# Kernel tuning notes

Hardware: AMD Instinct MI355X
Metric: run time of the kernel (lower is better)

## Reference

```python
import jax, jax.numpy as jnp
import numpy as np

N = 30000      # num nodes
E = 960000     # num edges (avg degree 32)
IN_DIM = 2048  # raw input feature dim
N_EMBED = 64
N_HID1 = 32
N_HID2 = 16
NUM_ET = 64    # num edge types (relations)
NUM_BASE = 16  # num bases for basis decomposition


def setup_inputs() -> dict:
    key = jax.random.key(0)
    ks = jax.random.split(key, 14)
    x = jax.random.normal(ks[0], (N, IN_DIM), jnp.float32)
    edge_index = jax.random.randint(ks[1], (2, E), 0, N, dtype=jnp.int32)
    edge_type = jnp.sort(jax.random.randint(ks[2], (E,), 0, NUM_ET, dtype=jnp.int32))
    # range_list[r] = [start, end) of relation r's edges (edge_type is sorted)
    bounds = jnp.searchsorted(edge_type, jnp.arange(NUM_ET + 1, dtype=jnp.int32))
    range_list = jnp.stack([bounds[:-1], bounds[1:]], axis=1)
    x_norm = jax.random.uniform(ks[3], (N,), jnp.float32, 0.5, 1.5)
    s = 0.1  # param init scale
    embed = jax.random.normal(ks[4], (IN_DIM, N_EMBED), jnp.float32)  # .normal_() in reset
    basis1 = jax.random.normal(ks[5], (NUM_BASE, N_EMBED, N_HID1), jnp.float32) * s
    att1 = jax.random.normal(ks[6], (NUM_ET, NUM_BASE), jnp.float32) * s
    root1 = jax.random.normal(ks[7], (N_EMBED, N_HID1), jnp.float32) * s
    bias1 = jnp.zeros((N_HID1,), jnp.float32)
    basis2 = jax.random.normal(ks[8], (NUM_BASE, N_HID1, N_HID2), jnp.float32) * s
    att2 = jax.random.normal(ks[9], (NUM_ET, NUM_BASE), jnp.float32) * s
    root2 = jax.random.normal(ks[10], (N_HID1, N_HID2), jnp.float32) * s
    bias2 = jnp.zeros((N_HID2,), jnp.float32)
    return dict(x=x, edge_index=edge_index, edge_type=edge_type, range_list=range_list,
                x_norm=x_norm, embed=embed, basis1=basis1, att1=att1, root1=root1,
                bias1=bias1, basis2=basis2, att2=att2, root2=root2, bias2=bias2)


def rgcn_layer(x, edge_index, edge_type, basis, att, root, bias):
    # basis-decomposed relation weights: W[r] = sum_b att[r,b] * basis[b]
    W = jnp.einsum('rb,bio->rio', att, basis)            # [R, in, out]
    # transform all nodes under every relation (R small per-relation GEMMs fused)
    H = jnp.einsum('ni,rio->rno', x, W)                  # [R, N, out]
    src, dst = edge_index[0], edge_index[1]
    msg = H[edge_type, src]                              # [E, out] gather per-edge message
    agg = jax.ops.segment_sum(msg, dst, num_segments=x.shape[0])  # scatter-add to targets
    return agg + x @ root + bias


def reference(x, edge_index, edge_type, range_list, x_norm,
              embed, basis1, att1, root1, bias1, basis2, att2, root2, bias2):
    h = (x @ embed) / x_norm[:, None]                    # embed matmul + norm
    h = jax.nn.relu(rgcn_layer(h, edge_index, edge_type, basis1, att1, root1, bias1))
    h = jax.nn.relu(rgcn_layer(h, edge_index, edge_type, basis2, att2, root2, bias2))
    return h
```

## Files before the change

### kernel.cpp

```cpp
#include <hip/hip_runtime.h>
#include <hip/hip_bf16.h>

#define NN   30000
#define EE   960000
#define IND  2048
#define NEMB 64
#define NH1  32
#define NH2  16
#define NET  64
#define NB   16

typedef __bf16 bf8 __attribute__((ext_vector_type(8)));
typedef __bf16 bf4 __attribute__((ext_vector_type(4)));
typedef __bf16 bf2 __attribute__((ext_vector_type(2)));
typedef float  f4  __attribute__((ext_vector_type(4)));

#define AS3 __attribute__((address_space(3)))
#define AS1 __attribute__((address_space(1)))

__device__ __forceinline__ void gll16(const void* g, void* l) {
    __builtin_amdgcn_global_load_lds((const AS1 unsigned int*)g,
                                     (AS3 unsigned int*)l, 16, 0, 0);
}

__device__ __forceinline__ bf8 bf8_zero() {
    bf8 z;
#pragma unroll
    for (int i = 0; i < 8; i++) z[i] = (__bf16)0.0f;
    return z;
}

__global__ __launch_bounds__(256) void k_prep(const float* __restrict__ embed,
                                              const float* __restrict__ basis1,
                                              const float* __restrict__ att1,
                                              const float* __restrict__ basis2,
                                              const float* __restrict__ att2,
                                              __bf16* __restrict__ embT,
                                              __bf16* __restrict__ W1T,
                                              __bf16* __restrict__ W2T) {
    int b = blockIdx.x;
    if (b < 512) {
        int idx = b * 256 + threadIdx.x;
        int n = idx >> 11, k = idx & 2047;
        embT[idx] = (__bf16)embed[k * NEMB + n];
    } else if (b < 576) {
        int r = b - 512;
        __shared__ float a[NB];
        if (threadIdx.x < NB) a[threadIdx.x] = att1[r * NB + threadIdx.x];
        __syncthreads();
        for (int idx = threadIdx.x; idx < NH1 * NEMB; idx += 256) {
            int o = idx >> 6, i = idx & 63;
            float acc = 0.f;
#pragma unroll
            for (int bb = 0; bb < NB; bb++) acc += a[bb] * basis1[(bb * NEMB + i) * NH1 + o];
            W1T[r * (NH1 * NEMB) + idx] = (__bf16)acc;
        }
    } else {
        int r = b - 576;
        __shared__ float a[NB];
        if (threadIdx.x < NB) a[threadIdx.x] = att2[r * NB + threadIdx.x];
        __syncthreads();
        for (int idx = threadIdx.x; idx < NH2 * NH1; idx += 256) {
            int o = idx >> 5, i = idx & 31;
            float acc = 0.f;
#pragma unroll
            for (int bb = 0; bb < NB; bb++) acc += a[bb] * basis2[(bb * NH1 + i) * NH2 + o];
            W2T[r * (NH2 * NH1) + idx] = (__bf16)acc;
        }
    }
}

__global__ __launch_bounds__(256) void k_gemm(const float* __restrict__ x,
                                              const float* __restrict__ xnorm,
                                              const __bf16* __restrict__ embT,
                                              const float* __restrict__ root1,
                                              const float* __restrict__ bias1,
                                              __bf16* __restrict__ h0b,
                                              float* __restrict__ out1) {
    __shared__ __align__(16) float  As[2][32 * 128];
    __shared__ __align__(16) __bf16 Bs[2][64 * 128];
    int t = threadIdx.x;
    int wv = t >> 6, lane = t & 63;
    int l15 = lane & 15, kg = lane >> 4;
    int rowbase = blockIdx.x * 32;
    int half = lane >> 5;
    int bslot = lane & 31;
    int q16 = lane >> 4;
    int slot16 = lane & 15;
    int n = wv * 16 + l15;
    int nswz = (n & 7) << 4;
    int aswz = (l15 & 7) << 4;
    f4 acc0 = (f4)0.0f, acc1 = (f4)0.0f;

    auto STAGE = [&](int c, int buf) {
#pragma unroll
        for (int i = 0; i < 4; i++) {
            int rp = wv * 4 + i;
            int row = rp * 2 + half;
            int grow = rowbase + row;
            if (grow >= NN) grow = NN - 1;
            const char* g = (const char*)x + (size_t)grow * (IND * 4) + c * 512
                          + ((bslot * 16) ^ ((row & 7) << 4));
            gll16(g, (char*)&As[buf][0] + rp * 1024);
        }
#pragma unroll
        for (int i = 0; i < 4; i++) {
            int rp = wv * 4 + i;
            int row = rp * 4 + q16;
            const char* g = (const char*)embT + (size_t)row * (IND * 2) + c * 256
                          + ((slot16 * 16) ^ ((row & 7) << 4));
            gll16(g, (char*)&Bs[buf][0] + rp * 1024);
        }
    };

    STAGE(0, 0);
    for (int c = 0; c < 16; c++) {
        int buf = c & 1;
        if (c < 15) {
            STAGE(c + 1, buf ^ 1);
            asm volatile("s_waitcnt vmcnt(8)" ::: "memory");
        } else {
            asm volatile("s_waitcnt vmcnt(0)" ::: "memory");
        }
        __builtin_amdgcn_s_barrier();
        __builtin_amdgcn_sched_barrier(0);
        const char* bsrow  = (const char*)&Bs[buf][0] + n * 256;
        const char* asrow0 = (const char*)&As[buf][0] + l15 * 512;
        const char* asrow1 = (const char*)&As[buf][0] + (l15 + 16) * 512;
#pragma unroll
        for (int kk = 0; kk < 4; kk++) {
            int aoff = ((kk * 128 + kg * 32) ^ aswz);
            float4 lo0 = *(const float4*)(asrow0 + aoff);
            float4 hi0 = *(const float4*)(asrow0 + (aoff ^ 16));
            float4 lo1 = *(const float4*)(asrow1 + aoff);
            float4 hi1 = *(const float4*)(asrow1 + (aoff ^ 16));
            bf8 b = *(const bf8*)(bsrow + ((kk * 64 + kg * 16) ^ nswz));
            bf8 a0, a1;
            a0[0]=(__bf16)lo0.x; a0[1]=(__bf16)lo0.y; a0[2]=(__bf16)lo0.z; a0[3]=(__bf16)lo0.w;
            a0[4]=(__bf16)hi0.x; a0[5]=(__bf16)hi0.y; a0[6]=(__bf16)hi0.z; a0[7]=(__bf16)hi0.w;
            a1[0]=(__bf16)lo1.x; a1[1]=(__bf16)lo1.y; a1[2]=(__bf16)lo1.z; a1[3]=(__bf16)lo1.w;
            a1[4]=(__bf16)hi1.x; a1[5]=(__bf16)hi1.y; a1[6]=(__bf16)hi1.z; a1[7]=(__bf16)hi1.w;
            acc0 = __builtin_amdgcn_mfma_f32_16x16x32_bf16(a0, b, acc0, 0, 0, 0);
            acc1 = __builtin_amdgcn_mfma_f32_16x16x32_bf16(a1, b, acc1, 0, 0, 0);
        }
        __builtin_amdgcn_sched_barrier(0);
        __builtin_amdgcn_s_barrier();
    }
    __bf16* h0s = (__bf16*)&As[0][0];
#pragma unroll
    for (int j = 0; j < 4; j++) {
        int lr0 = kg * 4 + j, lr1 = lr0 + 16;
        int r0 = rowbase + lr0, r1 = rowbase + lr1;
        float v0 = 0.f, v1 = 0.f;
        if (r0 < NN) v0 = acc0[j] / xnorm[r0];
        if (r1 < NN) v1 = acc1[j] / xnorm[r1];
        __bf16 b0 = (__bf16)v0, b1 = (__bf16)v1;
        if (r0 < NN) h0b[(size_t)r0 * NEMB + n] = b0;
        if (r1 < NN) h0b[(size_t)r1 * NEMB + n] = b1;
        h0s[lr0 * NEMB + n] = b0;
        h0s[lr1 * NEMB + n] = b1;
    }
    __syncthreads();
    {
        int row = t >> 3, c0 = (t & 7) * 4;
        int grow = rowbase + row;
        if (grow < NN) {
            const __bf16* hr = h0s + row * NEMB;
            float4 acc = *(const float4*)(bias1 + c0);
#pragma unroll
            for (int k = 0; k < NEMB; k++) {
                float a = (float)hr[k];
                float4 w = *(const float4*)(root1 + k * NH1 + c0);
                acc.x += a * w.x; acc.y += a * w.y;
                acc.z += a * w.z; acc.w += a * w.w;
            }
            *(float4*)(out1 + (size_t)grow * NH1 + c0) = acc;
        }
    }
}

__global__ __launch_bounds__(256) void k_edge1(const int* __restrict__ ei,
                                               const int* __restrict__ et,
                                               const __bf16* __restrict__ h0b,
                                               const __bf16* __restrict__ W1T,
                                               float* __restrict__ out1) {
    int wave = threadIdx.x >> 6, lane = threadIdx.x & 63;
    int l15 = lane & 15, kg = lane >> 4;
    int wid = blockIdx.x * 4 + wave;
    int er0 = wid * 32 + l15, er1 = er0 + 16;
    int et0v = et[er0],  et1v = et[er1];
    int src0 = ei[er0],  src1 = ei[er1];
    int dst0 = ei[EE + er0], dst1 = ei[EE + er1];
    const __bf16* hp0 = h0b + (size_t)src0 * NEMB + kg * 8;
    const __bf16* hp1 = h0b + (size_t)src1 * NEMB + kg * 8;
    bf8 a00 = *(const bf8*)hp0;
    bf8 a01 = *(const bf8*)(hp0 + 32);
    bf8 a10 = *(const bf8*)hp1;
    bf8 a11 = *(const bf8*)(hp1 + 32);
    bf8 zero = bf8_zero();
#pragma unroll
    for (int b = 0; b < 2; b++) {
        int my_et = b ? et1v : et0v;
        int my_dst = b ? dst1 : dst0;
        bf8 a0 = b ? a10 : a00;
        bf8 a1 = b ? a11 : a01;
        f4 c0 = (f4)0.0f, c1 = (f4)0.0f;
        int pos = 0;
        while (pos < 16) {
            int r = __shfl(my_et, pos);
            unsigned long long bl = __ballot(my_et == r);
            unsigned m16 = (unsigned)(bl & 0xFFFFull);
            int run = __builtin_ctz(~(m16 >> pos));
            int end = pos + run;
            const __bf16* wb = W1T + (size_t)r * (NH1 * NEMB) + (size_t)l15 * NEMB + kg * 8;
            bf8 b00 = *(const bf8*)(wb);
            bf8 b01 = *(const bf8*)(wb + 32);
            bf8 b10 = *(const bf8*)(wb + 16 * NEMB);
            bf8 b11 = *(const bf8*)(wb + 16 * NEMB + 32);
            bool use = (l15 >= pos) && (l15 < end);
            bf8 ua0 = use ? a0 : zero;
            bf8 ua1 = use ? a1 : zero;
            c0 = __builtin_amdgcn_mfma_f32_16x16x32_bf16(ua0, b00, c0, 0, 0, 0);
            c0 = __builtin_amdgcn_mfma_f32_16x16x32_bf16(ua1, b01, c0, 0, 0, 0);
            c1 = __builtin_amdgcn_mfma_f32_16x16x32_bf16(ua0, b10, c1, 0, 0, 0);
            c1 = __builtin_amdgcn_mfma_f32_16x16x32_bf16(ua1, b11, c1, 0, 0, 0);
            pos = end;
        }
#pragma unroll
        for (int j = 0; j < 4; j++) {
            int eidx = kg * 4 + j;
            int dst = __shfl(my_dst, eidx);
            atomicAdd(out1 + (size_t)dst * NH1 + l15,      c0[j]);
            atomicAdd(out1 + (size_t)dst * NH1 + 16 + l15, c1[j]);
        }
    }
}

__global__ __launch_bounds__(256) void k_mid(const float* __restrict__ out1,
                                             const float* __restrict__ root2,
                                             const float* __restrict__ bias2,
                                             __bf16* __restrict__ h1b,
                                             float* __restrict__ out) {
    int t = threadIdx.x;
    int row = blockIdx.x * 16 + (t >> 4);
    int col = t & 15;
    const float* orow = out1 + (size_t)row * NH1;
    float h[NH1];
#pragma unroll
    for (int k = 0; k < NH1; k++) h[k] = fmaxf(orow[k], 0.f);
    bf2 hb;
    hb[0] = (__bf16)h[2 * col];
    hb[1] = (__bf16)h[2 * col + 1];
    *(bf2*)(h1b + (size_t)row * NH1 + 2 * col) = hb;
    float acc = bias2[col];
#pragma unroll
    for (int k = 0; k < NH1; k++) acc += h[k] * root2[k * NH2 + col];
    out[(size_t)row * NH2 + col] = acc;
}

__global__ __launch_bounds__(256) void k_edge2(const int* __restrict__ ei,
                                               const int* __restrict__ et,
                                               const __bf16* __restrict__ h1b,
                                               const __bf16* __restrict__ W2T,
                                               float* __restrict__ out) {
    int wave = threadIdx.x >> 6, lane = threadIdx.x & 63;
    int l15 = lane & 15, kg = lane >> 4;
    int wid = blockIdx.x * 4 + wave;
    int er0 = wid * 32 + l15, er1 = er0 + 16;
    int et0v = et[er0],  et1v = et[er1];
    int src0 = ei[er0],  src1 = ei[er1];
    int dst0 = ei[EE + er0], dst1 = ei[EE + er1];
    bf8 ab0 = *(const bf8*)(h1b + (size_t)src0 * NH1 + kg * 8);
    bf8 ab1 = *(const bf8*)(h1b + (size_t)src1 * NH1 + kg * 8);
    bf8 zero = bf8_zero();
#pragma unroll
    for (int b = 0; b < 2; b++) {
        int my_et = b ? et1v : et0v;
        int my_dst = b ? dst1 : dst0;
        bf8 a = b ? ab1 : ab0;
        f4 c = (f4)0.0f;
        int pos = 0;
        while (pos < 16) {
            int r = __shfl(my_et, pos);
            unsigned long long bl = __ballot(my_et == r);
            unsigned m16 = (unsigned)(bl & 0xFFFFull);
            int run = __builtin_ctz(~(m16 >> pos));
            int end = pos + run;
            bf8 bb = *(const bf8*)(W2T + (size_t)r * (NH2 * NH1) + (size_t)l15 * NH1 + kg * 8);
            bool use = (l15 >= pos) && (l15 < end);
            c = __builtin_amdgcn_mfma_f32_16x16x32_bf16(use ? a : zero, bb, c, 0, 0, 0);
            pos = end;
        }
#pragma unroll
        for (int j = 0; j < 4; j++) {
            int eidx = kg * 4 + j;
            int dst = __shfl(my_dst, eidx);
            atomicAdd(out + (size_t)dst * NH2 + l15, c[j]);
        }
    }
}

__global__ __launch_bounds__(256) void k_relu2(float* __restrict__ o) {
    int i = blockIdx.x * 256 + threadIdx.x;
    if (i >= NN * NH2 / 4) return;
    float4 v = ((float4*)o)[i];
    v.x = fmaxf(v.x, 0.f); v.y = fmaxf(v.y, 0.f);
    v.z = fmaxf(v.z, 0.f); v.w = fmaxf(v.w, 0.f);
    ((float4*)o)[i] = v;
}

extern "C" void kernel_launch(void* const* d_in, const int* in_sizes, int n_in,
                              void* d_out, int out_size, void* d_ws, size_t ws_size,
                              hipStream_t stream) {
    const float* x      = (const float*)d_in[0];
    const int*   ei     = (const int*)d_in[1];
    const int*   et     = (const int*)d_in[2];
    const float* xnorm  = (const float*)d_in[4];
    const float* embed  = (const float*)d_in[5];
    const float* basis1 = (const float*)d_in[6];
    const float* att1   = (const float*)d_in[7];
    const float* root1  = (const float*)d_in[8];
    const float* bias1  = (const float*)d_in[9];
    const float* basis2 = (const float*)d_in[10];
    const float* att2   = (const float*)d_in[11];
    const float* root2  = (const float*)d_in[12];
    const float* bias2  = (const float*)d_in[13];
    float* out = (float*)d_out;

    char* ws = (char*)d_ws;
    __bf16* embT = (__bf16*)(ws + 0);
    __bf16* W1T  = (__bf16*)(ws + 262144);
    __bf16* W2T  = (__bf16*)(ws + 524288);
    __bf16* h0b  = (__bf16*)(ws + 589824);
    float*  out1 = (float*) (ws + 4429824);
    __bf16* h1b  = (__bf16*)(ws + 8269824);

    k_prep <<<640,  256, 0, stream>>>(embed, basis1, att1, basis2, att2, embT, W1T, W2T);
    k_gemm <<<938,  256, 0, stream>>>(x, xnorm, embT, root1, bias1, h0b, out1);
    k_edge1<<<7500, 256, 0, stream>>>(ei, et, h0b, W1T, out1);
    k_mid  <<<1875, 256, 0, stream>>>(out1, root2, bias2, h1b, out);
    k_edge2<<<7500, 256, 0, stream>>>(ei, et, h1b, W2T, out);
    k_relu2<<<469,  256, 0, stream>>>(out);
}
```

Baseline: 255.1 us.

## Merge prep+gemm and mid+edge2+relu into persistent kernels with grid barriers

Fuses the weight-prep and embed GEMM into one persistent kernel of 512 blocks separated by a software grid barrier, and likewise fuses the mid transform, second edge layer and final ReLU into one persistent kernel with two grid barriers. This removes several kernel launches and their inter-kernel gaps. In exchange the GEMM now runs 938 tiles over only 512 blocks, which leaves a tail round, and the spin barrier depends on all 512 blocks being co-resident (launch_bounds 256,2 across 256 CUs). The persistent loops also lower parallelism for the edge phase.

```diff
diff --git a/kernel.cpp b/kernel.cpp
--- a/kernel.cpp
+++ b/kernel.cpp
@@ -9,6 +9,7 @@
 #define NH2  16
 #define NET  64
 #define NB   16
+#define NBLKC 512
 
 typedef __bf16 bf8 __attribute__((ext_vector_type(8)));
 typedef __bf16 bf4 __attribute__((ext_vector_type(4)));
@@ -30,59 +31,72 @@
     return z;
 }
 
-__global__ __launch_bounds__(256) void k_prep(const float* __restrict__ embed,
-                                              const float* __restrict__ basis1,
-                                              const float* __restrict__ att1,
-                                              const float* __restrict__ basis2,
-                                              const float* __restrict__ att2,
-                                              __bf16* __restrict__ embT,
-                                              __bf16* __restrict__ W1T,
-                                              __bf16* __restrict__ W2T) {
-    int b = blockIdx.x;
-    if (b < 512) {
-        int idx = b * 256 + threadIdx.x;
-        int n = idx >> 11, k = idx & 2047;
-        embT[idx] = (__bf16)embed[k * NEMB + n];
-    } else if (b < 576) {
-        int r = b - 512;
-        __shared__ float a[NB];
-        if (threadIdx.x < NB) a[threadIdx.x] = att1[r * NB + threadIdx.x];
-        __syncthreads();
-        for (int idx = threadIdx.x; idx < NH1 * NEMB; idx += 256) {
-            int o = idx >> 6, i = idx & 63;
-            float acc = 0.f;
-#pragma unroll
-            for (int bb = 0; bb < NB; bb++) acc += a[bb] * basis1[(bb * NEMB + i) * NH1 + o];
-            W1T[r * (NH1 * NEMB) + idx] = (__bf16)acc;
-        }
-    } else {
-        int r = b - 576;
-        __shared__ float a[NB];
-        if (threadIdx.x < NB) a[threadIdx.x] = att2[r * NB + threadIdx.x];
-        __syncthreads();
-        for (int idx = threadIdx.x; idx < NH2 * NH1; idx += 256) {
-            int o = idx >> 5, i = idx & 31;
-            float acc = 0.f;
-#pragma unroll
-            for (int bb = 0; bb < NB; bb++) acc += a[bb] * basis2[(bb * NH1 + i) * NH2 + o];
-            W2T[r * (NH2 * NH1) + idx] = (__bf16)acc;
-        }
-    }
-}
-
-__global__ __launch_bounds__(256) void k_gemm(const float* __restrict__ x,
-                                              const float* __restrict__ xnorm,
-                                              const __bf16* __restrict__ embT,
-                                              const float* __restrict__ root1,
-                                              const float* __restrict__ bias1,
-                                              __bf16* __restrict__ h0b,
-                                              float* __restrict__ out1) {
+__device__ __forceinline__ void gridbar(int* bar, int target) {
+    __syncthreads();
+    if (threadIdx.x == 0) {
+        __threadfence();
+        if (atomicAdd(&bar[0], 1) == NBLKC - 1) {
+            bar[0] = 0;
+            __threadfence();
+            atomicAdd(&bar[1], 1);
+        }
+        while (__hip_atomic_load(&bar[1], __ATOMIC_ACQUIRE,
+                                 __HIP_MEMORY_SCOPE_AGENT) < target)
+            __builtin_amdgcn_s_sleep(32);
+        __threadfence();
+    }
+    __syncthreads();
+}
+
+__global__ __launch_bounds__(256, 2) void k_prep_gemm(
+        const float* __restrict__ embed, const float* __restrict__ basis1,
+        const float* __restrict__ att1, const float* __restrict__ basis2,
+        const float* __restrict__ att2, const float* __restrict__ x,
+        const float* __restrict__ xnorm, const float* __restrict__ root1,
+        const float* __restrict__ bias1,
+        __bf16* __restrict__ embT, __bf16* __restrict__ W1T, __bf16* __restrict__ W2T,
+        __bf16* __restrict__ h0b, float* __restrict__ out1, int* __restrict__ bar) {
     __shared__ __align__(16) float  As[2][32 * 128];
     __shared__ __align__(16) __bf16 Bs[2][64 * 128];
     int t = threadIdx.x;
     int wv = t >> 6, lane = t & 63;
     int l15 = lane & 15, kg = lane >> 4;
-    int rowbase = blockIdx.x * 32;
+
+    for (int vb = blockIdx.x; vb < 640; vb += NBLKC) {
+        if (vb < 512) {
+            int idx = vb * 256 + t;
+            int n = idx >> 11, k = idx & 2047;
+            embT[idx] = (__bf16)embed[k * NEMB + n];
+        } else if (vb < 576) {
+            int r = vb - 512;
+            float* a = (float*)&As[0][0];
+            if (t < NB) a[t] = att1[r * NB + t];
+            __syncthreads();
+            for (int idx = t; idx < NH1 * NEMB; idx += 256) {
+                int o = idx >> 6, i = idx & 63;
+                float acc = 0.f;
+#pragma unroll
+                for (int bb = 0; bb < NB; bb++) acc += a[bb] * basis1[(bb * NEMB + i) * NH1 + o];
+                W1T[r * (NH1 * NEMB) + idx] = (__bf16)acc;
+            }
+            __syncthreads();
+        } else {
+            int r = vb - 576;
+            float* a = (float*)&As[0][0];
+            if (t < NB) a[t] = att2[r * NB + t];
+            __syncthreads();
+            for (int idx = t; idx < NH2 * NH1; idx += 256) {
+                int o = idx >> 5, i = idx & 31;
+                float acc = 0.f;
+#pragma unroll
+                for (int bb = 0; bb < NB; bb++) acc += a[bb] * basis2[(bb * NH1 + i) * NH2 + o];
+                W2T[r * (NH2 * NH1) + idx] = (__bf16)acc;
+            }
+            __syncthreads();
+        }
+    }
+    gridbar(bar, 1);
+
     int half = lane >> 5;
     int bslot = lane & 31;
     int q16 = lane >> 4;
@@ -90,92 +104,97 @@
     int n = wv * 16 + l15;
     int nswz = (n & 7) << 4;
     int aswz = (l15 & 7) << 4;
-    f4 acc0 = (f4)0.0f, acc1 = (f4)0.0f;
-
-    auto STAGE = [&](int c, int buf) {
-#pragma unroll
-        for (int i = 0; i < 4; i++) {
-            int rp = wv * 4 + i;
-            int row = rp * 2 + half;
+
+    for (int vt = blockIdx.x; vt < 938; vt += NBLKC) {
+        int rowbase = vt * 32;
+        f4 acc0 = (f4)0.0f, acc1 = (f4)0.0f;
+
+        auto STAGE = [&](int c, int buf) {
+#pragma unroll
+            for (int i = 0; i < 4; i++) {
+                int rp = wv * 4 + i;
+                int row = rp * 2 + half;
+                int grow = rowbase + row;
+                if (grow >= NN) grow = NN - 1;
+                const char* g = (const char*)x + (size_t)grow * (IND * 4) + c * 512
+                              + ((bslot * 16) ^ ((row & 7) << 4));
+                gll16(g, (char*)&As[buf][0] + rp * 1024);
+            }
+#pragma unroll
+            for (int i = 0; i < 4; i++) {
+                int rp = wv * 4 + i;
+                int row = rp * 4 + q16;
+                const char* g = (const char*)embT + (size_t)row * (IND * 2) + c * 256
+                              + ((slot16 * 16) ^ ((row & 7) << 4));
+                gll16(g, (char*)&Bs[buf][0] + rp * 1024);
+            }
+        };
+
+        STAGE(0, 0);
+        for (int c = 0; c < 16; c++) {
+            int buf = c & 1;
+            if (c < 15) {
+                STAGE(c + 1, buf ^ 1);
+                asm volatile("s_waitcnt vmcnt(8)" ::: "memory");
+            } else {
+                asm volatile("s_waitcnt vmcnt(0)" ::: "memory");
+            }
+            __builtin_amdgcn_s_barrier();
+            __builtin_amdgcn_sched_barrier(0);
+            const char* bsrow  = (const char*)&Bs[buf][0] + n * 256;
+            const char* asrow0 = (const char*)&As[buf][0] + l15 * 512;
+            const char* asrow1 = (const char*)&As[buf][0] + (l15 + 16) * 512;
+#pragma unroll
+            for (int kk = 0; kk < 4; kk++) {
+                int aoff = ((kk * 128 + kg * 32) ^ aswz);
+                float4 lo0 = *(const float4*)(asrow0 + aoff);
+                float4 hi0 = *(const float4*)(asrow0 + (aoff ^ 16));
+                float4 lo1 = *(const float4*)(asrow1 + aoff);
+                float4 hi1 = *(const float4*)(asrow1 + (aoff ^ 16));
+                bf8 b = *(const bf8*)(bsrow + ((kk * 64 + kg * 16) ^ nswz));
+                bf8 a0, a1;
+                a0[0]=(__bf16)lo0.x; a0[1]=(__bf16)lo0.y; a0[2]=(__bf16)lo0.z; a0[3]=(__bf16)lo0.w;
+                a0[4]=(__bf16)hi0.x; a0[5]=(__bf16)hi0.y; a0[6]=(__bf16)hi0.z; a0[7]=(__bf16)hi0.w;
+                a1[0]=(__bf16)lo1.x; a1[1]=(__bf16)lo1.y; a1[2]=(__bf16)lo1.z; a1[3]=(__bf16)lo1.w;
+                a1[4]=(__bf16)hi1.x; a1[5]=(__bf16)hi1.y; a1[6]=(__bf16)hi1.z; a1[7]=(__bf16)hi1.w;
+                acc0 = __builtin_amdgcn_mfma_f32_16x16x32_bf16(a0, b, acc0, 0, 0, 0);
+                acc1 = __builtin_amdgcn_mfma_f32_16x16x32_bf16(a1, b, acc1, 0, 0, 0);
+            }
+            __builtin_amdgcn_sched_barrier(0);
+            __builtin_amdgcn_s_barrier();
+        }
+        __bf16* h0s = (__bf16*)&As[0][0];
+#pragma unroll
+        for (int j = 0; j < 4; j++) {
+            int lr0 = kg * 4 + j, lr1 = lr0 + 16;
+            int r0 = rowbase + lr0, r1 = rowbase + lr1;
+            float v0 = 0.f, v1 = 0.f;
+            if (r0 < NN) v0 = acc0[j] / xnorm[r0];
+            if (r1 < NN) v1 = acc1[j] / xnorm[r1];
+            __bf16 b0 = (__bf16)v0, b1 = (__bf16)v1;
+            if (r0 < NN) h0b[(size_t)r0 * NEMB + n] = b0;
+            if (r1 < NN) h0b[(size_t)r1 * NEMB + n] = b1;
+            h0s[lr0 * NEMB + n] = b0;
+            h0s[lr1 * NEMB + n] = b1;
+        }
+        __syncthreads();
+        {
+            int row = t >> 3, c0 = (t & 7) * 4;
             int grow = rowbase + row;
-            if (grow >= NN) grow = NN - 1;
-            const char* g = (const char*)x + (size_t)grow * (IND * 4) + c * 512
-                          + ((bslot * 16) ^ ((row & 7) << 4));
-            gll16(g, (char*)&As[buf][0] + rp * 1024);
-        }
-#pragma unroll
-        for (int i = 0; i < 4; i++) {
-            int rp = wv * 4 + i;
-            int row = rp * 4 + q16;
-            const char* g = (const char*)embT + (size_t)row * (IND * 2) + c * 256
-                          + ((slot16 * 16) ^ ((row & 7) << 4));
-            gll16(g, (char*)&Bs[buf][0] + rp * 1024);
-        }
-    };
-
-    STAGE(0, 0);
-    for (int c = 0; c < 16; c++) {
-        int buf = c & 1;
-        if (c < 15) {
-            STAGE(c + 1, buf ^ 1);
-            asm volatile("s_waitcnt vmcnt(8)" ::: "memory");
-        } else {
-            asm volatile("s_waitcnt vmcnt(0)" ::: "memory");
-        }
-        __builtin_amdgcn_s_barrier();
-        __builtin_amdgcn_sched_barrier(0);
-        const char* bsrow  = (const char*)&Bs[buf][0] + n * 256;
-        const char* asrow0 = (const char*)&As[buf][0] + l15 * 512;
-        const char* asrow1 = (const char*)&As[buf][0] + (l15 + 16) * 512;
-#pragma unroll
-        for (int kk = 0; kk < 4; kk++) {
-            int aoff = ((kk * 128 + kg * 32) ^ aswz);
-            float4 lo0 = *(const float4*)(asrow0 + aoff);
-            float4 hi0 = *(const float4*)(asrow0 + (aoff ^ 16));
-            float4 lo1 = *(const float4*)(asrow1 + aoff);
-            float4 hi1 = *(const float4*)(asrow1 + (aoff ^ 16));
-            bf8 b = *(const bf8*)(bsrow + ((kk * 64 + kg * 16) ^ nswz));
-            bf8 a0, a1;
-            a0[0]=(__bf16)lo0.x; a0[1]=(__bf16)lo0.y; a0[2]=(__bf16)lo0.z; a0[3]=(__bf16)lo0.w;
-            a0[4]=(__bf16)hi0.x; a0[5]=(__bf16)hi0.y; a0[6]=(__bf16)hi0.z; a0[7]=(__bf16)hi0.w;
-            a1[0]=(__bf16)lo1.x; a1[1]=(__bf16)lo1.y; a1[2]=(__bf16)lo1.z; a1[3]=(__bf16)lo1.w;
-            a1[4]=(__bf16)hi1.x; a1[5]=(__bf16)hi1.y; a1[6]=(__bf16)hi1.z; a1[7]=(__bf16)hi1.w;
-            acc0 = __builtin_amdgcn_mfma_f32_16x16x32_bf16(a0, b, acc0, 0, 0, 0);
-            acc1 = __builtin_amdgcn_mfma_f32_16x16x32_bf16(a1, b, acc1, 0, 0, 0);
-        }
-        __builtin_amdgcn_sched_barrier(0);
-        __builtin_amdgcn_s_barrier();
-    }
-    __bf16* h0s = (__bf16*)&As[0][0];
-#pragma unroll
-    for (int j = 0; j < 4; j++) {
-        int lr0 = kg * 4 + j, lr1 = lr0 + 16;
-        int r0 = rowbase + lr0, r1 = rowbase + lr1;
-        float v0 = 0.f, v1 = 0.f;
-        if (r0 < NN) v0 = acc0[j] / xnorm[r0];
-        if (r1 < NN) v1 = acc1[j] / xnorm[r1];
-        __bf16 b0 = (__bf16)v0, b1 = (__bf16)v1;
-        if (r0 < NN) h0b[(size_t)r0 * NEMB + n] = b0;
-        if (r1 < NN) h0b[(size_t)r1 * NEMB + n] = b1;
-        h0s[lr0 * NEMB + n] = b0;
-        h0s[lr1 * NEMB + n] = b1;
-    }
-    __syncthreads();
-    {
-        int row = t >> 3, c0 = (t & 7) * 4;
-        int grow = rowbase + row;
-        if (grow < NN) {
-            const __bf16* hr = h0s + row * NEMB;
-            float4 acc = *(const float4*)(bias1 + c0);
-#pragma unroll
-            for (int k = 0; k < NEMB; k++) {
-                float a = (float)hr[k];
-                float4 w = *(const float4*)(root1 + k * NH1 + c0);
-                acc.x += a * w.x; acc.y += a * w.y;
-                acc.z += a * w.z; acc.w += a * w.w;
-            }
-            *(float4*)(out1 + (size_t)grow * NH1 + c0) = acc;
-        }
+            if (grow < NN) {
+                const __bf16* hr = h0s + row * NEMB;
+                float4 acc = *(const float4*)(bias1 + c0);
+#pragma unroll
+                for (int k = 0; k < NEMB; k++) {
+                    float a = (float)hr[k];
+                    float4 w = *(const float4*)(root1 + k * NH1 + c0);
+                    acc.x += a * w.x; acc.y += a * w.y;
+                    acc.z += a * w.z; acc.w += a * w.w;
+                }
+                *(float4*)(out1 + (size_t)grow * NH1 + c0) = acc;
+            }
+        }
+        __syncthreads();
     }
 }
 
@@ -236,77 +255,81 @@
     }
 }
 
-__global__ __launch_bounds__(256) void k_mid(const float* __restrict__ out1,
-                                             const float* __restrict__ root2,
-                                             const float* __restrict__ bias2,
-                                             __bf16* __restrict__ h1b,
-                                             float* __restrict__ out) {
+__global__ __launch_bounds__(256, 2) void k_tail(const int* __restrict__ ei,
+                                                 const int* __restrict__ et,
+                                                 const float* __restrict__ out1,
+                                                 const float* __restrict__ root2,
+                                                 const float* __restrict__ bias2,
+                                                 const __bf16* __restrict__ W2T,
+                                                 __bf16* __restrict__ h1b,
+                                                 float* __restrict__ out,
+                                                 int* __restrict__ bar) {
     int t = threadIdx.x;
-    int row = blockIdx.x * 16 + (t >> 4);
-    int col = t & 15;
-    const float* orow = out1 + (size_t)row * NH1;
-    float h[NH1];
-#pragma unroll
-    for (int k = 0; k < NH1; k++) h[k] = fmaxf(orow[k], 0.f);
-    bf2 hb;
-    hb[0] = (__bf16)h[2 * col];
-    hb[1] = (__bf16)h[2 * col + 1];
-    *(bf2*)(h1b + (size_t)row * NH1 + 2 * col) = hb;
-    float acc = bias2[col];
-#pragma unroll
-    for (int k = 0; k < NH1; k++) acc += h[k] * root2[k * NH2 + col];
-    out[(size_t)row * NH2 + col] = acc;
-}
-
-__global__ __launch_bounds__(256) void k_edge2(const int* __restrict__ ei,
-                                               const int* __restrict__ et,
-                                               const __bf16* __restrict__ h1b,
-                                               const __bf16* __restrict__ W2T,
-                                               float* __restrict__ out) {
-    int wave = threadIdx.x >> 6, lane = threadIdx.x & 63;
+    int wv = t >> 6, lane = t & 63;
     int l15 = lane & 15, kg = lane >> 4;
-    int wid = blockIdx.x * 4 + wave;
-    int er0 = wid * 32 + l15, er1 = er0 + 16;
-    int et0v = et[er0],  et1v = et[er1];
-    int src0 = ei[er0],  src1 = ei[er1];
-    int dst0 = ei[EE + er0], dst1 = ei[EE + er1];
-    bf8 ab0 = *(const bf8*)(h1b + (size_t)src0 * NH1 + kg * 8);
-    bf8 ab1 = *(const bf8*)(h1b + (size_t)src1 * NH1 + kg * 8);
-    bf8 zero = bf8_zero();
-#pragma unroll
-    for (int b = 0; b < 2; b++) {
-        int my_et = b ? et1v : et0v;
-        int my_dst = b ? dst1 : dst0;
-        bf8 a = b ? ab1 : ab0;
-        f4 c = (f4)0.0f;
-        int pos = 0;
-        while (pos < 16) {
-            int r = __shfl(my_et, pos);
-            unsigned long long bl = __ballot(my_et == r);
-            unsigned m16 = (unsigned)(bl & 0xFFFFull);
-            int run = __builtin_ctz(~(m16 >> pos));
-            int end = pos + run;
-            bf8 bb = *(const bf8*)(W2T + (size_t)r * (NH2 * NH1) + (size_t)l15 * NH1 + kg * 8);
-            bool use = (l15 >= pos) && (l15 < end);
-            c = __builtin_amdgcn_mfma_f32_16x16x32_bf16(use ? a : zero, bb, c, 0, 0, 0);
-            pos = end;
-        }
-#pragma unroll
-        for (int j = 0; j < 4; j++) {
-            int eidx = kg * 4 + j;
-            int dst = __shfl(my_dst, eidx);
-            atomicAdd(out + (size_t)dst * NH2 + l15, c[j]);
-        }
-    }
-}
-
-__global__ __launch_bounds__(256) void k_relu2(float* __restrict__ o) {
-    int i = blockIdx.x * 256 + threadIdx.x;
-    if (i >= NN * NH2 / 4) return;
-    float4 v = ((float4*)o)[i];
-    v.x = fmaxf(v.x, 0.f); v.y = fmaxf(v.y, 0.f);
-    v.z = fmaxf(v.z, 0.f); v.w = fmaxf(v.w, 0.f);
-    ((float4*)o)[i] = v;
+
+    for (int rb = blockIdx.x; rb < 1875; rb += NBLKC) {
+        int row = rb * 16 + (t >> 4);
+        int col = t & 15;
+        const float* orow = out1 + (size_t)row * NH1;
+        float h[NH1];
+#pragma unroll
+        for (int k = 0; k < NH1; k++) h[k] = fmaxf(orow[k], 0.f);
+        bf2 hb;
+        hb[0] = (__bf16)h[2 * col];
+        hb[1] = (__bf16)h[2 * col + 1];
+        *(bf2*)(h1b + (size_t)row * NH1 + 2 * col) = hb;
+        float acc = bias2[col];
+#pragma unroll
+        for (int k = 0; k < NH1; k++) acc += h[k] * root2[k * NH2 + col];
+        out[(size_t)row * NH2 + col] = acc;
+    }
+    gridbar(bar, 1);
+
+    {
+        bf8 zero = bf8_zero();
+        for (int wid = blockIdx.x * 4 + wv; wid < NN; wid += NBLKC * 4) {
+            int er0 = wid * 32 + l15, er1 = er0 + 16;
+            int et0v = et[er0],  et1v = et[er1];
+            int src0 = ei[er0],  src1 = ei[er1];
+            int dst0 = ei[EE + er0], dst1 = ei[EE + er1];
+            bf8 ab0 = *(const bf8*)(h1b + (size_t)src0 * NH1 + kg * 8);
+            bf8 ab1 = *(const bf8*)(h1b + (size_t)src1 * NH1 + kg * 8);
+#pragma unroll
+            for (int s = 0; s < 2; s++) {
+                int my_et = s ? et1v : et0v;
+                int my_dst = s ? dst1 : dst0;
+                bf8 a = s ? ab1 : ab0;
+                f4 c = (f4)0.0f;
+                int pos = 0;
+                while (pos < 16) {
+                    int r = __shfl(my_et, pos);
+                    unsigned long long bl = __ballot(my_et == r);
+                    unsigned m16 = (unsigned)(bl & 0xFFFFull);
+                    int run = __builtin_ctz(~(m16 >> pos));
+                    int end = pos + run;
+                    bf8 bb = *(const bf8*)(W2T + (size_t)r * (NH2 * NH1) + (size_t)l15 * NH1 + kg * 8);
+                    bool use = (l15 >= pos) && (l15 < end);
+                    c = __builtin_amdgcn_mfma_f32_16x16x32_bf16(use ? a : zero, bb, c, 0, 0, 0);
+                    pos = end;
+                }
+#pragma unroll
+                for (int j = 0; j < 4; j++) {
+                    int eidx = kg * 4 + j;
+                    int dst = __shfl(my_dst, eidx);
+                    atomicAdd(out + (size_t)dst * NH2 + l15, c[j]);
+                }
+            }
+        }
+    }
+    gridbar(bar, 2);
+
+    for (int i = blockIdx.x * 256 + t; i < NN * NH2 / 4; i += NBLKC * 256) {
+        float4 v = ((float4*)out)[i];
+        v.x = fmaxf(v.x, 0.f); v.y = fmaxf(v.y, 0.f);
+        v.z = fmaxf(v.z, 0.f); v.w = fmaxf(v.w, 0.f);
+        ((float4*)out)[i] = v;
+    }
 }
 
 extern "C" void kernel_launch(void* const* d_in, const int* in_sizes, int n_in,
@@ -334,11 +357,14 @@
     __bf16* h0b  = (__bf16*)(ws + 589824);
     float*  out1 = (float*) (ws + 4429824);
     __bf16* h1b  = (__bf16*)(ws + 8269824);
-
-    k_prep <<<640,  256, 0, stream>>>(embed, basis1, att1, basis2, att2, embT, W1T, W2T);
-    k_gemm <<<938,  256, 0, stream>>>(x, xnorm, embT, root1, bias1, h0b, out1);
-    k_edge1<<<7500, 256, 0, stream>>>(ei, et, h0b, W1T, out1);
-    k_mid  <<<1875, 256, 0, stream>>>(out1, root2, bias2, h1b, out);
-    k_edge2<<<7500, 256, 0, stream>>>(ei, et, h1b, W2T, out);
-    k_relu2<<<469,  256, 0, stream>>>(out);
-}
+    int*    bar1 = (int*)   (ws + 10189824);
+    int*    bar2 = (int*)   (ws + 10189856);
+
+    hipMemsetAsync(bar1, 0, 64, stream);
+    k_prep_gemm<<<NBLKC, 256, 0, stream>>>(embed, basis1, att1, basis2, att2, x,
+                                           xnorm, root1, bias1,
+                                           embT, W1T, W2T, h0b, out1, bar1);
+    k_edge1    <<<7500,  256, 0, stream>>>(ei, et, h0b, W1T, out1);
+    k_tail     <<<NBLKC, 256, 0, stream>>>(ei, et, out1, root2, bias2, W2T,
+                                           h1b, out, bar2);
+}
```

Result: slower. 767.8 us (+200.9%).

## Enlarge embed GEMM tile to 64 rows with 512 threads, single-buffered LDS

Applied to the files above, without the earlier changes.

The embedding GEMM now processes 64 rows per block with 8 waves in a 4x2 layout, so each staged embT tile serves twice as many rows. The explicit double-buffered global_load_lds prefetch pipeline is dropped in favour of a single buffer with __syncthreads around each chunk. The goal is to cut redundant B traffic and raise waves per CU through a smaller per-wave LDS footprint. The trade-off is that load latency is no longer overlapped inside a block and must be hidden by other resident waves. The normalisation now multiplies by a reciprocal instead of dividing.

```diff
diff --git a/kernel.cpp b/kernel.cpp
--- a/kernel.cpp
+++ b/kernel.cpp
@@ -70,29 +70,34 @@
     }
 }
 
-__global__ __launch_bounds__(256) void k_gemm(const float* __restrict__ x,
+__global__ __launch_bounds__(512) void k_gemm(const float* __restrict__ x,
                                               const float* __restrict__ xnorm,
                                               const __bf16* __restrict__ embT,
                                               const float* __restrict__ root1,
                                               const float* __restrict__ bias1,
                                               __bf16* __restrict__ h0b,
                                               float* __restrict__ out1) {
-    __shared__ __align__(16) float  As[2][32 * 128];
-    __shared__ __align__(16) __bf16 Bs[2][64 * 128];
+    __shared__ __align__(16) float  As[64 * 128];
+    __shared__ __align__(16) __bf16 Bs[64 * 128];
     int t = threadIdx.x;
     int wv = t >> 6, lane = t & 63;
     int l15 = lane & 15, kg = lane >> 4;
-    int rowbase = blockIdx.x * 32;
+    int rowbase = blockIdx.x * 64;
+    int wr = wv >> 1, wc = wv & 1;
     int half = lane >> 5;
     int bslot = lane & 31;
     int q16 = lane >> 4;
     int slot16 = lane & 15;
-    int n = wv * 16 + l15;
-    int nswz = (n & 7) << 4;
-    int aswz = (l15 & 7) << 4;
+    int arow_l = wr * 16 + l15;
+    int aswz = (arow_l & 7) << 4;
+    int n0 = wc * 32 + l15, n1 = n0 + 16;
+    int nswz0 = (n0 & 7) << 4, nswz1 = (n1 & 7) << 4;
+    const char* asrow  = (const char*)As + arow_l * 512;
+    const char* bsrow0 = (const char*)Bs + n0 * 256;
+    const char* bsrow1 = (const char*)Bs + n1 * 256;
     f4 acc0 = (f4)0.0f, acc1 = (f4)0.0f;
 
-    auto STAGE = [&](int c, int buf) {
+    for (int c = 0; c < 16; c++) {
 #pragma unroll
         for (int i = 0; i < 4; i++) {
             int rp = wv * 4 + i;
@@ -101,64 +106,50 @@
             if (grow >= NN) grow = NN - 1;
             const char* g = (const char*)x + (size_t)grow * (IND * 4) + c * 512
                           + ((bslot * 16) ^ ((row & 7) << 4));
-            gll16(g, (char*)&As[buf][0] + rp * 1024);
-        }
-#pragma unroll
-        for (int i = 0; i < 4; i++) {
-            int rp = wv * 4 + i;
+            gll16(g, (char*)As + rp * 1024);
+        }
+#pragma unroll
+        for (int i = 0; i < 2; i++) {
+            int rp = wv * 2 + i;
             int row = rp * 4 + q16;
             const char* g = (const char*)embT + (size_t)row * (IND * 2) + c * 256
                           + ((slot16 * 16) ^ ((row & 7) << 4));
-            gll16(g, (char*)&Bs[buf][0] + rp * 1024);
-        }
-    };
-
-    STAGE(0, 0);
-    for (int c = 0; c < 16; c++) {
-        int buf = c & 1;
-        if (c < 15) {
-            STAGE(c + 1, buf ^ 1);
-            asm volatile("s_waitcnt vmcnt(8)" ::: "memory");
-        } else {
-            asm volatile("s_waitcnt vmcnt(0)" ::: "memory");
-        }
-        __builtin_amdgcn_s_barrier();
-        __builtin_amdgcn_sched_barrier(0);
-        const char* bsrow  = (const char*)&Bs[buf][0] + n * 256;
-        const char* asrow0 = (const char*)&As[buf][0] + l15 * 512;
-        const char* asrow1 = (const char*)&As[buf][0] + (l15 + 16) * 512;
+            gll16(g, (char*)Bs + rp * 1024);
+        }
+        __syncthreads();
 #pragma unroll
         for (int kk = 0; kk < 4; kk++) {
             int aoff = ((kk * 128 + kg * 32) ^ aswz);
-            float4 lo0 = *(const float4*)(asrow0 + aoff);
-            float4 hi0 = *(const float4*)(asrow0 + (aoff ^ 16));
-            float4 lo1 = *(const float4*)(asrow1 + aoff);
-            float4 hi1 = *(const float4*)(asrow1 + (aoff ^ 16));
-            bf8 b = *(const bf8*)(bsrow + ((kk * 64 + kg * 16) ^ nswz));
-            bf8 a0, a1;
-            a0[0]=(__bf16)lo0.x; a0[1]=(__bf16)lo0.y; a0[2]=(__bf16)lo0.z; a0[3]=(__bf16)lo0.w;
-            a0[4]=(__bf16)hi0.x; a0[5]=(__bf16)hi0.y; a0[6]=(__bf16)hi0.z; a0[7]=(__bf16)hi0.w;
-            a1[0]=(__bf16)lo1.x; a1[1]=(__bf16)lo1.y; a1[2]=(__bf16)lo1.z; a1[3]=(__bf16)lo1.w;
-            a1[4]=(__bf16)hi1.x; a1[5]=(__bf16)hi1.y; a1[6]=(__bf16)hi1.z; a1[7]=(__bf16)hi1.w;
-            acc0 = __builtin_amdgcn_mfma_f32_16x16x32_bf16(a0, b, acc0, 0, 0, 0);
-            acc1 = __builtin_amdgcn_mfma_f32_16x16x32_bf16(a1, b, acc1, 0, 0, 0);
-        }
-        __builtin_amdgcn_sched_barrier(0);
-        __builtin_amdgcn_s_barrier();
-    }
-    __bf16* h0s = (__bf16*)&As[0][0];
+            float4 lo = *(const float4*)(asrow + aoff);
+            float4 hi = *(const float4*)(asrow + (aoff ^ 16));
+            bf8 b0 = *(const bf8*)(bsrow0 + ((kk * 64 + kg * 16) ^ nswz0));
+            bf8 b1 = *(const bf8*)(bsrow1 + ((kk * 64 + kg * 16) ^ nswz1));
+            bf8 a;
+            a[0]=(__bf16)lo.x; a[1]=(__bf16)lo.y; a[2]=(__bf16)lo.z; a[3]=(__bf16)lo.w;
+            a[4]=(__bf16)hi.x; a[5]=(__bf16)hi.y; a[6]=(__bf16)hi.z; a[7]=(__bf16)hi.w;
+            acc0 = __builtin_amdgcn_mfma_f32_16x16x32_bf16(a, b0, acc0, 0, 0, 0);
+            acc1 = __builtin_amdgcn_mfma_f32_16x16x32_bf16(a, b1, acc1, 0, 0, 0);
+        }
+        __syncthreads();
+    }
+    __bf16* h0s = (__bf16*)As;
 #pragma unroll
     for (int j = 0; j < 4; j++) {
-        int lr0 = kg * 4 + j, lr1 = lr0 + 16;
-        int r0 = rowbase + lr0, r1 = rowbase + lr1;
+        int lr = wr * 16 + kg * 4 + j;
+        int r = rowbase + lr;
         float v0 = 0.f, v1 = 0.f;
-        if (r0 < NN) v0 = acc0[j] / xnorm[r0];
-        if (r1 < NN) v1 = acc1[j] / xnorm[r1];
+        if (r < NN) {
+            float inv = 1.0f / xnorm[r];
+            v0 = acc0[j] * inv;
+            v1 = acc1[j] * inv;
+        }
         __bf16 b0 = (__bf16)v0, b1 = (__bf16)v1;
-        if (r0 < NN) h0b[(size_t)r0 * NEMB + n] = b0;
-        if (r1 < NN) h0b[(size_t)r1 * NEMB + n] = b1;
-        h0s[lr0 * NEMB + n] = b0;
-        h0s[lr1 * NEMB + n] = b1;
+        if (r < NN) {
+            h0b[(size_t)r * NEMB + n0] = b0;
+            h0b[(size_t)r * NEMB + n1] = b1;
+        }
+        h0s[lr * NEMB + n0] = b0;
+        h0s[lr * NEMB + n1] = b1;
     }
     __syncthreads();
     {
@@ -336,7 +327,7 @@
     __bf16* h1b  = (__bf16*)(ws + 8269824);
 
     k_prep <<<640,  256, 0, stream>>>(embed, basis1, att1, basis2, att2, embT, W1T, W2T);
-    k_gemm <<<938,  256, 0, stream>>>(x, xnorm, embT, root1, bias1, h0b, out1);
+    k_gemm <<<469,  512, 0, stream>>>(x, xnorm, embT, root1, bias1, h0b, out1);
     k_edge1<<<7500, 256, 0, stream>>>(ei, et, h0b, W1T, out1);
     k_mid  <<<1875, 256, 0, stream>>>(out1, root2, bias2, h1b, out);
     k_edge2<<<7500, 256, 0, stream>>>(ei, et, h1b, W2T, out);
```

Measured after the change: 229.9 us. 9.9% less time.
